# Kernel tuning notes

Measured on AMD Instinct MI355X. Metric: run time of the kernel, lower is better.

Reference implementation:

```python
import jax, jax.numpy as jnp
import numpy as np

NUM_BUSES = 128
N = NUM_BUSES - 1            # non-slack buses
BATCH = 4096
NUM_CS = 200                 # charging stations
S_BASE = 1000.0
MAX_CS_POWER = 22.17
MIN_CS_POWER = -22.17
MAX_EV_CH = 22.0
MAX_EV_DIS = -22.0
EV_CAP = 70.0
EV_MIN_CAP = 15.0
TIMESCALE_H = 15.0 / 60.0    # timescale minutes -> hours
ITERATIONS = 100
TOLERANCE = 1e-6
STATE_DIM = 4 + 2 * N + 3 * NUM_CS  # 858


def setup_inputs() -> dict:
    key = jax.random.key(0)
    k1, k2, k3, k4, k5, k6, k7 = jax.random.split(key, 7)
    action = jax.random.uniform(k1, (BATCH, NUM_CS), jnp.float32, -1.0, 1.0)
    state = jnp.zeros((BATCH, STATE_DIM), jnp.float32)
    # baseline active/reactive bus loads (kW / kvar), small vs s_base
    state = state.at[:, 4:4 + N].set(jax.random.uniform(k2, (BATCH, N), jnp.float32) * 50.0)
    state = state.at[:, 4 + N:4 + 2 * N].set(jax.random.uniform(k3, (BATCH, N), jnp.float32) * 10.0)
    ev_start = 4 + 2 * N
    cap = jax.random.uniform(k4, (BATCH, NUM_CS), jnp.float32) * EV_CAP
    bus = jax.random.randint(k5, (BATCH, NUM_CS), 0, N).astype(jnp.float32)
    state = state.at[:, ev_start:ev_start + 3 * NUM_CS:3].set(cap)
    state = state.at[:, ev_start + 2:ev_start + 2 + 3 * NUM_CS:3].set(bus)
    # power-flow matrices: K small-magnitude (contraction), Lm = flat-voltage vector
    K = ((jax.random.normal(k6, (N, N)) + 1j * jax.random.normal(k7, (N, N))) * 0.005).astype(jnp.complex64)
    L_param = jnp.ones((N, 1), jnp.complex64)
    return {"action": action, "state": state, "K": K, "L_param": L_param}


def _forward(action, state, K, L_param):
    B, C = action.shape
    ev_start = 4 + 2 * N
    cap = state[:, ev_start:ev_start + 3 * C:3]                 # (B, C)
    bus = state[:, ev_start + 2:ev_start + 2 + 3 * C:3].astype(jnp.int32)
    conn = (cap > 0).astype(action.dtype)
    max_ch = jnp.minimum(MAX_EV_CH, conn * (EV_CAP - cap) / TIMESCALE_H)
    max_dis = jnp.maximum(MAX_EV_DIS, conn * (EV_MIN_CAP - cap) / TIMESCALE_H)
    pos = jnp.where(action >= 0, 1.0, 0.0)
    power = action * MAX_CS_POWER * pos - action * MIN_CS_POWER * (1.0 - pos)
    power = jnp.maximum(jnp.minimum(power, max_ch), max_dis)
    # scatter-add CS power onto buses (per batch row)
    ev_bus = jnp.zeros((B, N), power.dtype).at[jnp.arange(B)[:, None], bus].add(power)
    p_pu = (state[:, 4:4 + N] + ev_bus) / S_BASE
    q_pu = state[:, 4 + N:4 + 2 * N] / S_BASE
    S = (p_pu + 1j * q_pu).astype(K.dtype).T                    # (N, B) complex
    Lm = jnp.broadcast_to(L_param, (N, B))
    v_init = jnp.ones((N, B), K.dtype)

    # Z-bus fixed-point iteration with early-exit freeze (mirrors torch while loop)
    def step(carry, _):
        v0, done = carry
        Lc = jnp.conj(S / v0)
        v_k = K @ Lc + Lm                                       # (N, B)
        tol = jnp.max(jnp.abs(jnp.abs(v_k) - jnp.abs(v0)))
        v_new = jnp.where(done, v0, v_k)
        return (v_new, jnp.logical_or(done, tol < TOLERANCE)), None

    (v0, _), _ = jax.lax.scan(step, (v_init, jnp.array(False)), None, length=ITERATIONS)
    vmag = jnp.abs(v0).T                                        # (B, N) real
    loss = jnp.minimum(0.0, 0.05 - jnp.abs(1.0 - vmag))
    return 1000.0 * loss.sum(axis=1)                            # (B,)


def reference(action, state, K, L_param):
    return _forward(action, state, K, L_param)
```

## Files before the change

### kernel.cpp

```cpp
#include <hip/hip_runtime.h>
#include <math.h>

#define N_BUS 127
#define BATCH 4096
#define NUM_CS 200
#define STATE_DIM 858
#define EV_START 258
#define COLS 16
#define NITER 5

typedef __attribute__((ext_vector_type(8))) short short8;
typedef __attribute__((ext_vector_type(4))) short short4v;
typedef __attribute__((ext_vector_type(4))) float f32x4;

static __device__ __forceinline__ short f2bf(float f) {
    unsigned u = __float_as_uint(f);
    return (short)((u + 0x7FFFu + ((u >> 16) & 1u)) >> 16);
}

__global__ __launch_bounds__(512, 4) void vvl_main(const float* __restrict__ action,
                                                   const float* __restrict__ state,
                                                   const float2* __restrict__ K,
                                                   const float2* __restrict__ Lp,
                                                   float* __restrict__ out) {
    __shared__ float sq[COLS][258];
    __shared__ __align__(16) short B8[2][2][4][4][COLS][8];
    __shared__ float lossred[COLS];

    const int tid = threadIdx.x;
    const int w  = tid >> 6;
    const int l  = tid & 63;
    const int cc = l & 15;
    const int g  = l >> 4;
    const int b0 = blockIdx.x * COLS;
    const int col = tid >> 5;
    const int j   = tid & 31;

    const float*  st_row_c = state + (size_t)(b0 + col) * STATE_DIM;
    const float2* st2      = (const float2*)(st_row_c + 4);
    const float*  act_row  = action + (size_t)(b0 + col) * NUM_CS;

    float2 pqv[4];
    #pragma unroll
    for (int jj = 0; jj < 4; ++jj) {
        int idx = j + 32 * jj; idx = idx < 127 ? idx : 126;
        pqv[jj] = st2[idx];
    }
    float av[7], capv[7], busv[7];
    #pragma unroll
    for (int kk = 0; kk < 7; ++kk) {
        int cs = j + 32 * kk; int csc = cs < NUM_CS ? cs : NUM_CS - 1;
        av[kk]   = act_row[csc];
        capv[kk] = st_row_c[EV_START + 3 * csc];
        busv[kk] = st_row_c[EV_START + 2 + 3 * csc];
    }
    const int arow = 16 * w + (l & 15);
    const bool rok = arow < N_BUS;
    const float2* Krow = K + (size_t)(rok ? arow : 0) * N_BUS;
    float2 k1[16];
    #pragma unroll
    for (int kt = 0; kt < 2; ++kt)
        #pragma unroll
        for (int i = 0; i < 8; ++i) {
            int k = 32 * kt + 8 * g + i;
            k1[kt * 8 + i] = Krow[k < N_BUS ? k : 0];
        }

    if (tid < COLS) lossred[tid] = 0.0f;
    #pragma unroll
    for (int jj = 0; jj < 4; ++jj) {
        int idx = j + 32 * jj;
        if (idx < 127) *(float2*)&sq[col][2 * idx] = pqv[jj];
    }
    __syncthreads();

    #pragma unroll
    for (int kk = 0; kk < 7; ++kk) {
        int cs = j + 32 * kk;
        float cap  = capv[kk];
        float conn = (cap > 0.0f) ? 1.0f : 0.0f;
        float mch  = fminf(22.0f,  conn * (70.0f - cap) * 4.0f);
        float mds  = fmaxf(-22.0f, conn * (15.0f - cap) * 4.0f);
        float pw   = fmaxf(fminf(av[kk] * 22.17f, mch), mds);
        int bi = (int)busv[kk];
        bi = bi < 0 ? 0 : (bi > N_BUS - 1 ? N_BUS - 1 : bi);
        if (cs < NUM_CS) atomicAdd(&sq[col][bi], pw);
    }

    float2 k2[16];
    #pragma unroll
    for (int kt = 2; kt < 4; ++kt)
        #pragma unroll
        for (int i = 0; i < 8; ++i) {
            int k = 32 * kt + 8 * g + i;
            k2[(kt - 2) * 8 + i] = Krow[k < N_BUS ? k : 0];
        }

    short8 AKr[4], AKi[4];
    #pragma unroll
    for (int kt = 0; kt < 2; ++kt)
        #pragma unroll
        for (int i = 0; i < 8; ++i) {
            int k = 32 * kt + 8 * g + i;
            bool ok = rok && (k < N_BUS);
            float2 e = k1[kt * 8 + i];
            AKr[kt][i] = f2bf(ok ? e.x : 0.0f);
            AKi[kt][i] = f2bf(ok ? e.y : 0.0f);
        }

    __syncthreads();

    float Sr[4], Si[4], lmr[4], lmi[4], vr[4], vi[4];
    #pragma unroll
    for (int r = 0; r < 4; ++r) {
        int row = 16 * w + 4 * g + r;
        if (row < N_BUS) {
            Sr[r] = sq[cc][row] * 1e-3f;
            Si[r] = sq[cc][127 + row] * 1e-3f;
            float2 lp = Lp[row];
            lmr[r] = lp.x; lmi[r] = lp.y;
        } else {
            Sr[r] = 0.0f; Si[r] = 0.0f; lmr[r] = 1.0f; lmi[r] = 0.0f;
        }
        vr[r] = 1.0f; vi[r] = 0.0f;
    }

    #pragma unroll
    for (int kt = 2; kt < 4; ++kt)
        #pragma unroll
        for (int i = 0; i < 8; ++i) {
            int k = 32 * kt + 8 * g + i;
            bool ok = rok && (k < N_BUS);
            float2 e = k2[(kt - 2) * 8 + i];
            AKr[kt][i] = f2bf(ok ? e.x : 0.0f);
            AKi[kt][i] = f2bf(ok ? e.y : 0.0f);
        }

    const int k0  = 16 * w + 4 * g;
    const int ktw = k0 >> 5;
    const int gi  = (k0 >> 3) & 3;
    const int i0  = k0 & 7;

    for (int it = 0; it < NITER; ++it) {
        const int buf = it & 1;
        short4v pr, pi;
        #pragma unroll
        for (int r = 0; r < 4; ++r) {
            float d   = vr[r] * vr[r] + vi[r] * vi[r];
            float inv = __builtin_amdgcn_rcpf(d);
            pr[r] = f2bf((Sr[r] * vr[r] + Si[r] * vi[r]) * inv);
            pi[r] = f2bf((Sr[r] * vi[r] - Si[r] * vr[r]) * inv);
        }
        *(short4v*)&B8[buf][0][ktw][gi][cc][i0] = pr;
        *(short4v*)&B8[buf][1][ktw][gi][cc][i0] = pi;
        __syncthreads();

        f32x4 are = {0.f, 0.f, 0.f, 0.f}, aim = {0.f, 0.f, 0.f, 0.f};
        #pragma unroll
        for (int kt = 0; kt < 4; ++kt) {
            short8 Br  = *(const short8*)&B8[buf][0][kt][g][cc][0];
            short8 Bi8 = *(const short8*)&B8[buf][1][kt][g][cc][0];
            aim = __builtin_amdgcn_mfma_f32_16x16x32_bf16(AKr[kt], Bi8, aim, 0, 0, 0);
            aim = __builtin_amdgcn_mfma_f32_16x16x32_bf16(AKi[kt], Br,  aim, 0, 0, 0);
            are = __builtin_amdgcn_mfma_f32_16x16x32_bf16(AKr[kt], Br,  are, 0, 0, 0);
            #pragma unroll
            for (int i = 0; i < 8; ++i) Bi8[i] = Bi8[i] ^ (short)0x8000;
            are = __builtin_amdgcn_mfma_f32_16x16x32_bf16(AKi[kt], Bi8, are, 0, 0, 0);
        }
        #pragma unroll
        for (int r = 0; r < 4; ++r) {
            vr[r] = are[r] + lmr[r];
            vi[r] = aim[r] + lmi[r];
        }
    }

    float ls = 0.0f;
    #pragma unroll
    for (int r = 0; r < 4; ++r) {
        int row = 16 * w + 4 * g + r;
        if (row < N_BUS) {
            float na = sqrtf(vr[r] * vr[r] + vi[r] * vi[r]);
            ls += fminf(0.0f, 0.05f - fabsf(1.0f - na));
        }
    }
    ls += __shfl_xor(ls, 16);
    ls += __shfl_xor(ls, 32);
    if (g == 0) atomicAdd(&lossred[cc], ls);
    __syncthreads();
    if (tid < COLS) out[b0 + tid] = 1000.0f * lossred[tid];
}

extern "C" void kernel_launch(void* const* d_in, const int* in_sizes, int n_in,
                              void* d_out, int out_size, void* d_ws, size_t ws_size,
                              hipStream_t stream) {
    const float*  action = (const float*)d_in[0];
    const float*  state  = (const float*)d_in[1];
    const float2* K      = (const float2*)d_in[2];
    const float2* Lp     = (const float2*)d_in[3];
    float* out = (float*)d_out;

    vvl_main<<<BATCH / COLS, 512, 0, stream>>>(action, state, K, Lp, out);
}
```

Before: 17.04 us.

## Load all K row tiles upfront and relax launch bounds occupancy hint

Issues all 32 K-row loads at the start of the kernel instead of splitting them into two phases around the scatter-add, then converts them to bf16 in one loop. The launch-bounds minimum-blocks hint drops from 4 to 2, giving the compiler more registers to hold the larger set of in-flight loads. The aim is more memory-level parallelism and less latency exposure in the prologue. The cost is higher register pressure and possibly lower occupancy per CU. The LDS array is renamed, which changes nothing.

```diff
diff --git a/kernel.cpp b/kernel.cpp
--- a/kernel.cpp
+++ b/kernel.cpp
@@ -18,13 +18,13 @@
     return (short)((u + 0x7FFFu + ((u >> 16) & 1u)) >> 16);
 }
 
-__global__ __launch_bounds__(512, 4) void vvl_main(const float* __restrict__ action,
+__global__ __launch_bounds__(512, 2) void vvl_main(const float* __restrict__ action,
                                                    const float* __restrict__ state,
                                                    const float2* __restrict__ K,
                                                    const float2* __restrict__ Lp,
                                                    float* __restrict__ out) {
     __shared__ float sq[COLS][258];
-    __shared__ __align__(16) short B8[2][2][4][4][COLS][8];
+    __shared__ __align__(16) short B8s[2][2][4][4][COLS][8];
     __shared__ float lossred[COLS];
 
     const int tid = threadIdx.x;
@@ -57,16 +57,17 @@
     const int arow = 16 * w + (l & 15);
     const bool rok = arow < N_BUS;
     const float2* Krow = K + (size_t)(rok ? arow : 0) * N_BUS;
-    float2 k1[16];
+    float2 kv[32];
     #pragma unroll
-    for (int kt = 0; kt < 2; ++kt)
+    for (int kt = 0; kt < 4; ++kt)
         #pragma unroll
         for (int i = 0; i < 8; ++i) {
             int k = 32 * kt + 8 * g + i;
-            k1[kt * 8 + i] = Krow[k < N_BUS ? k : 0];
+            kv[kt * 8 + i] = Krow[k < N_BUS ? k : 0];
         }
 
     if (tid < COLS) lossred[tid] = 0.0f;
+
     #pragma unroll
     for (int jj = 0; jj < 4; ++jj) {
         int idx = j + 32 * jj;
@@ -87,23 +88,14 @@
         if (cs < NUM_CS) atomicAdd(&sq[col][bi], pw);
     }
 
-    float2 k2[16];
-    #pragma unroll
-    for (int kt = 2; kt < 4; ++kt)
-        #pragma unroll
-        for (int i = 0; i < 8; ++i) {
-            int k = 32 * kt + 8 * g + i;
-            k2[(kt - 2) * 8 + i] = Krow[k < N_BUS ? k : 0];
-        }
-
     short8 AKr[4], AKi[4];
     #pragma unroll
-    for (int kt = 0; kt < 2; ++kt)
+    for (int kt = 0; kt < 4; ++kt)
         #pragma unroll
         for (int i = 0; i < 8; ++i) {
             int k = 32 * kt + 8 * g + i;
             bool ok = rok && (k < N_BUS);
-            float2 e = k1[kt * 8 + i];
+            float2 e = kv[kt * 8 + i];
             AKr[kt][i] = f2bf(ok ? e.x : 0.0f);
             AKi[kt][i] = f2bf(ok ? e.y : 0.0f);
         }
@@ -125,17 +117,6 @@
         vr[r] = 1.0f; vi[r] = 0.0f;
     }
 
-    #pragma unroll
-    for (int kt = 2; kt < 4; ++kt)
-        #pragma unroll
-        for (int i = 0; i < 8; ++i) {
-            int k = 32 * kt + 8 * g + i;
-            bool ok = rok && (k < N_BUS);
-            float2 e = k2[(kt - 2) * 8 + i];
-            AKr[kt][i] = f2bf(ok ? e.x : 0.0f);
-            AKi[kt][i] = f2bf(ok ? e.y : 0.0f);
-        }
-
     const int k0  = 16 * w + 4 * g;
     const int ktw = k0 >> 5;
     const int gi  = (k0 >> 3) & 3;
@@ -151,15 +132,15 @@
             pr[r] = f2bf((Sr[r] * vr[r] + Si[r] * vi[r]) * inv);
             pi[r] = f2bf((Sr[r] * vi[r] - Si[r] * vr[r]) * inv);
         }
-        *(short4v*)&B8[buf][0][ktw][gi][cc][i0] = pr;
-        *(short4v*)&B8[buf][1][ktw][gi][cc][i0] = pi;
+        *(short4v*)&B8s[buf][0][ktw][gi][cc][i0] = pr;
+        *(short4v*)&B8s[buf][1][ktw][gi][cc][i0] = pi;
         __syncthreads();
 
         f32x4 are = {0.f, 0.f, 0.f, 0.f}, aim = {0.f, 0.f, 0.f, 0.f};
         #pragma unroll
         for (int kt = 0; kt < 4; ++kt) {
-            short8 Br  = *(const short8*)&B8[buf][0][kt][g][cc][0];
-            short8 Bi8 = *(const short8*)&B8[buf][1][kt][g][cc][0];
+            short8 Br  = *(const short8*)&B8s[buf][0][kt][g][cc][0];
+            short8 Bi8 = *(const short8*)&B8s[buf][1][kt][g][cc][0];
             aim = __builtin_amdgcn_mfma_f32_16x16x32_bf16(AKr[kt], Bi8, aim, 0, 0, 0);
             aim = __builtin_amdgcn_mfma_f32_16x16x32_bf16(AKi[kt], Br,  aim, 0, 0, 0);
             are = __builtin_amdgcn_mfma_f32_16x16x32_bf16(AKr[kt], Br,  are, 0, 0, 0);
```

Measured after the change: 17.96 us. +5.4%, slower.
